# Performance work log

Measured on AMD Instinct MI355X. Metric: run time of the kernel, lower is better.

## Reference

```python
import jax, jax.numpy as jnp
import numpy as np

N = 100000
E = 3200000
F_IN, F_HID, F_OUT = 512, 16, 40


def setup_inputs() -> dict:
    key = jax.random.key(0)
    k1, k2, k3, k4 = jax.random.split(key, 4)
    x = jax.random.normal(k1, (N, F_IN), dtype=jnp.float32)
    edge_index = jax.random.randint(k2, (2, E), 0, N, dtype=jnp.int64)
    # Glorot-style init for the two GCN layer weights + zero biases
    W1 = jax.random.normal(k3, (F_IN, F_HID), dtype=jnp.float32) / np.sqrt(F_IN)
    b1 = jnp.zeros((F_HID,), dtype=jnp.float32)
    W2 = jax.random.normal(k4, (F_HID, F_OUT), dtype=jnp.float32) / np.sqrt(F_HID)
    b2 = jnp.zeros((F_OUT,), dtype=jnp.float32)
    return {"x": x, "edge_index": edge_index, "W1": W1, "b1": b1, "W2": W2, "b2": b2}


def _gcn_conv(x, src, dst, W, b):
    # x' = D^{-1/2} (A + I) D^{-1/2} (x W) + b   (standard GCNConv with self-loops)
    n = x.shape[0]
    h = x @ W  # [N, F_out] -- transform first (cheap edge traffic)
    deg = jax.ops.segment_sum(jnp.ones_like(dst, dtype=h.dtype), dst, num_segments=n) + 1.0  # +1 self-loop
    dinv = jax.lax.rsqrt(deg)
    msgs = h[src] * (dinv[src] * dinv[dst])[:, None]  # [E, F_out]
    agg = jax.ops.segment_sum(msgs, dst, num_segments=n)
    agg = agg + h * (dinv * dinv)[:, None]  # self-loop contribution
    return agg + b


def reference(x, edge_index, W1, b1, W2, b2):
    src, dst = edge_index[0], edge_index[1]
    h = _gcn_conv(x, src, dst, W1, b1)
    h = jax.nn.relu(h)
    # dropout is identity in eval mode (training=False)
    h = _gcn_conv(h, src, dst, W2, b2)
    return jax.nn.log_softmax(h, axis=1)
```

## Files before the change

kernel.cpp:

```cpp
#include <hip/hip_runtime.h>
#include <hip/hip_fp16.h>
#include <math.h>

#define FIN 512
#define FH 16
#define FOUT 40
#define DT 448
#define SUB 512
#define SRC_BITS 17
#define SRC_MASK 0x1FFFF
#define BCHUNK 4096
#define HCHUNK 16384
#define NB_MAX 1024
#define AP 17
#define NTS_MAX 200

typedef unsigned int u32;

__device__ __forceinline__ void gload_lds16(const void* g, void* l) {
  __builtin_amdgcn_global_load_lds((const __attribute__((address_space(1))) u32*)g,
                                   (__attribute__((address_space(3))) u32*)l, 16, 0, 0);
}

__global__ __launch_bounds__(256) void histA_k(const int* __restrict__ dst, int E, int NB,
                                               unsigned* __restrict__ bcnt) {
  __shared__ unsigned h[NB_MAX];
  for (int b = threadIdx.x; b < NB; b += 256) h[b] = 0;
  __syncthreads();
  const int base = blockIdx.x * HCHUNK;
  const int cn = min(HCHUNK, E - base);
  for (int u = threadIdx.x; u < cn; u += 256)
    atomicAdd(&h[((unsigned)dst[base + u]) / DT], 1u);
  __syncthreads();
  for (int b = threadIdx.x; b < NB; b += 256) {
    unsigned c = h[b];
    if (c) atomicAdd(&bcnt[b], c);
  }
}

__global__ __launch_bounds__(1024) void scanB_k(const unsigned* __restrict__ bcnt, int NB,
                                                unsigned* __restrict__ boff,
                                                unsigned* __restrict__ bcur) {
  __shared__ unsigned ws[16];
  const int t = threadIdx.x, lane = t & 63, wid = t >> 6;
  unsigned v = (t < NB) ? bcnt[t] : 0;
  unsigned incl = v;
#pragma unroll
  for (int d = 1; d < 64; d <<= 1) {
    unsigned o = __shfl_up(incl, d);
    if (lane >= d) incl += o;
  }
  if (lane == 63) ws[wid] = incl;
  __syncthreads();
  unsigned woff = 0, tot = 0;
#pragma unroll
  for (int w = 0; w < 16; ++w) {
    unsigned s = ws[w];
    if (w < wid) woff += s;
    tot += s;
  }
  unsigned ex = woff + incl - v;
  if (t < NB) { boff[t] = ex; bcur[t] = ex; }
  if (t == 0) boff[NB] = tot;
}

__global__ __launch_bounds__(256) void bin_k(const int* __restrict__ src,
                                             const int* __restrict__ dst, int E, int NB,
                                             unsigned* __restrict__ bcur,
                                             unsigned* __restrict__ bins) {
  __shared__ unsigned hist[NB_MAX];
  __shared__ unsigned excl[NB_MAX];
  __shared__ unsigned gbase[NB_MAX];
  __shared__ unsigned lcur[NB_MAX];
  __shared__ unsigned stage[BCHUNK];
  __shared__ unsigned short sbkt[BCHUNK];
  __shared__ unsigned wtot[4];
  const int t = threadIdx.x, lane = t & 63, wid = t >> 6;
  for (int b = t; b < NB; b += 256) hist[b] = 0;
  __syncthreads();
  const int base = blockIdx.x * BCHUNK;
  const int cn = min(BCHUNK, E - base);
  for (int u = t; u < cn; u += 256)
    atomicAdd(&hist[((unsigned)dst[base + u]) / DT], 1u);
  __syncthreads();
  unsigned loc[4], s = 0;
#pragma unroll
  for (int j = 0; j < 4; ++j) {
    int idx = t * 4 + j;
    loc[j] = s;
    s += (idx < NB) ? hist[idx] : 0;
  }
  unsigned incl = s;
#pragma unroll
  for (int d = 1; d < 64; d <<= 1) {
    unsigned o = __shfl_up(incl, d);
    if (lane >= d) incl += o;
  }
  if (lane == 63) wtot[wid] = incl;
  __syncthreads();
  unsigned woff = 0;
  for (int w = 0; w < wid; ++w) woff += wtot[w];
  unsigned tex = woff + incl - s;
#pragma unroll
  for (int j = 0; j < 4; ++j) {
    int idx = t * 4 + j;
    if (idx < NB) excl[idx] = tex + loc[j];
  }
  __syncthreads();
  for (int b = t; b < NB; b += 256) {
    unsigned c = hist[b];
    gbase[b] = c ? atomicAdd(&bcur[b], c) : 0u;
    lcur[b] = excl[b];
  }
  __syncthreads();
  for (int u = t; u < cn; u += 256) {
    int e = base + u;
    unsigned d = (unsigned)dst[e];
    unsigned bkt = d / DT;
    unsigned dloc = d - bkt * DT;
    unsigned pk = ((unsigned)src[e]) | (dloc << SRC_BITS);
    unsigned lr = atomicAdd(&lcur[bkt], 1u);
    stage[lr] = pk;
    sbkt[lr] = (unsigned short)bkt;
  }
  __syncthreads();
  for (int u = t; u < cn; u += 256) {
    unsigned bkt = sbkt[u];
    bins[gbase[bkt] + (u - excl[bkt])] = stage[u];
  }
}

__global__ __launch_bounds__(512) void deg_k(const unsigned* __restrict__ boff,
                                             const unsigned* __restrict__ bins, int n,
                                             float* __restrict__ dinv) {
  __shared__ unsigned dh[DT];
  const int t = threadIdx.x, b = blockIdx.x;
  if (t < DT) dh[t] = 0;
  __syncthreads();
  const unsigned jb = boff[b], je = boff[b + 1];
  for (unsigned j = jb + t; j < je; j += 512) atomicAdd(&dh[bins[j] >> SRC_BITS], 1u);
  __syncthreads();
  const int i = b * DT + t;
  if (t < DT && i < n) dinv[i] = rsqrtf((float)dh[t] + 1.0f);
}

__global__ __launch_bounds__(1024) void bin2_k(const unsigned* __restrict__ boff,
                                               const unsigned* __restrict__ bins, int nts,
                                               unsigned* __restrict__ out2,
                                               unsigned* __restrict__ off2) {
  __shared__ unsigned h2[NTS_MAX];
  __shared__ unsigned o2[NTS_MAX + 1];
  __shared__ unsigned cur2[NTS_MAX];
  const int t = threadIdx.x, b = blockIdx.x;
  const unsigned jb = boff[b], je = boff[b + 1];
  if (t < nts) h2[t] = 0;
  __syncthreads();
  for (unsigned j = jb + t; j < je; j += 1024)
    atomicAdd(&h2[(bins[j] & SRC_MASK) >> 9], 1u);
  __syncthreads();
  if (t == 0) {
    unsigned s = 0;
    for (int i = 0; i < nts; ++i) { o2[i] = s; s += h2[i]; }
    o2[nts] = s;
  }
  __syncthreads();
  if (t < nts) cur2[t] = o2[t];
  if (t <= nts) off2[(size_t)b * (nts + 1) + t] = o2[t];
  __syncthreads();
  for (unsigned j = jb + t; j < je; j += 1024) {
    const unsigned pk = bins[j];
    const unsigned srcf = pk & SRC_MASK;
    const unsigned st = srcf >> 9;
    const unsigned p = atomicAdd(&cur2[st], 1u);
    out2[jb + p] = (srcf & 511u) | ((pk >> SRC_BITS) << 9);
  }
}

__global__ __launch_bounds__(256) void gemm1_k(const float* __restrict__ x,
                                               const float* __restrict__ W1,
                                               const float* __restrict__ dinv, int n,
                                               __half* __restrict__ hs1) {
  __shared__ float w1s[FIN * FH];
  for (int idx = threadIdx.x; idx < FIN * FH; idx += 256) w1s[idx] = W1[idx];
  __syncthreads();
  const int row_raw = blockIdx.x * 256 + threadIdx.x;
  const int row = row_raw < n ? row_raw : n - 1;
  const float4* __restrict__ xr = (const float4*)(x + (size_t)row * FIN);
  float4 a0 = {0, 0, 0, 0}, a1 = {0, 0, 0, 0}, a2 = {0, 0, 0, 0}, a3 = {0, 0, 0, 0};
#pragma unroll 2
  for (int it = 0; it < FIN / 4; ++it) {
    float4 xv = xr[it];
    const float* wf = w1s + it * 4 * FH;
#pragma unroll
    for (int j = 0; j < 4; ++j) {
      const float xj = (j == 0) ? xv.x : (j == 1) ? xv.y : (j == 2) ? xv.z : xv.w;
      const float* wj = wf + j * FH;
      float4 w0 = *(const float4*)(wj + 0);
      float4 w1 = *(const float4*)(wj + 4);
      float4 w2 = *(const float4*)(wj + 8);
      float4 w3 = *(const float4*)(wj + 12);
      a0.x += xj * w0.x; a0.y += xj * w0.y; a0.z += xj * w0.z; a0.w += xj * w0.w;
      a1.x += xj * w1.x; a1.y += xj * w1.y; a1.z += xj * w1.z; a1.w += xj * w1.w;
      a2.x += xj * w2.x; a2.y += xj * w2.y; a2.z += xj * w2.z; a2.w += xj * w2.w;
      a3.x += xj * w3.x; a3.y += xj * w3.y; a3.z += xj * w3.z; a3.w += xj * w3.w;
    }
  }
  if (row_raw < n) {
    const float di = dinv[row];
    __half2 hb[8];
    hb[0] = __floats2half2_rn(a0.x * di, a0.y * di);
    hb[1] = __floats2half2_rn(a0.z * di, a0.w * di);
    hb[2] = __floats2half2_rn(a1.x * di, a1.y * di);
    hb[3] = __floats2half2_rn(a1.z * di, a1.w * di);
    hb[4] = __floats2half2_rn(a2.x * di, a2.y * di);
    hb[5] = __floats2half2_rn(a2.z * di, a2.w * di);
    hb[6] = __floats2half2_rn(a3.x * di, a3.y * di);
    hb[7] = __floats2half2_rn(a3.z * di, a3.w * di);
    uint4* o = (uint4*)(hs1 + (size_t)row * FH);
    o[0] = ((const uint4*)hb)[0];
    o[1] = ((const uint4*)hb)[1];
  }
}

__device__ __forceinline__ void accum_row(float* __restrict__ arow, uint4 q0, uint4 q1) {
  float2 f;
  f = __half22float2(*(const __half2*)&q0.x); atomicAdd(arow + 0, f.x);  atomicAdd(arow + 1, f.y);
  f = __half22float2(*(const __half2*)&q0.y); atomicAdd(arow + 2, f.x);  atomicAdd(arow + 3, f.y);
  f = __half22float2(*(const __half2*)&q0.z); atomicAdd(arow + 4, f.x);  atomicAdd(arow + 5, f.y);
  f = __half22float2(*(const __half2*)&q0.w); atomicAdd(arow + 6, f.x);  atomicAdd(arow + 7, f.y);
  f = __half22float2(*(const __half2*)&q1.x); atomicAdd(arow + 8, f.x);  atomicAdd(arow + 9, f.y);
  f = __half22float2(*(const __half2*)&q1.y); atomicAdd(arow + 10, f.x); atomicAdd(arow + 11, f.y);
  f = __half22float2(*(const __half2*)&q1.z); atomicAdd(arow + 12, f.x); atomicAdd(arow + 13, f.y);
  f = __half22float2(*(const __half2*)&q1.w); atomicAdd(arow + 14, f.x); atomicAdd(arow + 15, f.y);
}

__device__ __forceinline__ void stage_sub(const __half* __restrict__ tab, int st,
                                          __half* __restrict__ buf, int t) {
  const __half* g = tab + ((size_t)st * SUB + (t >> 1)) * FH + (t & 1) * 8;
  gload_lds16(g, buf + t * 8);
}

__device__ __forceinline__ void consume_sub(const unsigned* __restrict__ out2, unsigned jb,
                                            unsigned a, unsigned e,
                                            const __half* __restrict__ buf,
                                            float* __restrict__ acc, int t) {
  for (unsigned j = a + t; j < e; j += 1024) {
    const unsigned pk = out2[jb + j];
    const int srcl = pk & 511, dstl = pk >> 9;
    const uint4 q0 = *(const uint4*)(buf + srcl * FH);
    const uint4 q1 = *(const uint4*)(buf + srcl * FH + 8);
    accum_row(acc + dstl * AP, q0, q1);
  }
}

__device__ __forceinline__ void tile_gather(const __half* __restrict__ tab,
                                            const unsigned* __restrict__ out2,
                                            const unsigned* __restrict__ off2r,
                                            unsigned jb, int nts, int t,
                                            __half* __restrict__ sb0,
                                            __half* __restrict__ sb1,
                                            float* __restrict__ acc) {
  for (int u = t; u < DT * AP; u += 1024) acc[u] = 0.f;
  stage_sub(tab, 0, sb0, t);
  __syncthreads();
  for (int st = 0; st < nts; ++st) {
    asm volatile("s_waitcnt vmcnt(0)" ::: "memory");
    __builtin_amdgcn_sched_barrier(0);
    __builtin_amdgcn_s_barrier();
    __builtin_amdgcn_sched_barrier(0);
    __half* cur = (st & 1) ? sb1 : sb0;
    __half* nxt = (st & 1) ? sb0 : sb1;
    if (st + 1 < nts) stage_sub(tab, st + 1, nxt, t);
    consume_sub(out2, jb, off2r[st], off2r[st + 1], cur, acc, t);
    __builtin_amdgcn_sched_barrier(0);
    __builtin_amdgcn_s_barrier();
    __builtin_amdgcn_sched_barrier(0);
  }
  __syncthreads();
}

__global__ __launch_bounds__(1024) void gath1_k(const __half* __restrict__ hs1,
                                                const unsigned* __restrict__ boff,
                                                const unsigned* __restrict__ out2,
                                                const unsigned* __restrict__ off2, int nts,
                                                const float* __restrict__ dinv,
                                                const float* __restrict__ b1, int n,
                                                __half* __restrict__ rs) {
  __shared__ float acc[DT * AP];
  __shared__ __half sb0[SUB * FH];
  __shared__ __half sb1[SUB * FH];
  __shared__ float b1s[FH];
  const int t = threadIdx.x, b = blockIdx.x;
  if (t < FH) b1s[t] = b1[t];
  tile_gather(hs1, out2, off2 + (size_t)b * (nts + 1), boff[b], nts, t, sb0, sb1, acc);
  const int base = b * DT;
  for (int idx = t; idx < DT * 4; idx += 1024) {
    const int node = idx >> 2, sub = idx & 3;
    const int i = base + node;
    if (i < n) {
      const float* arow = acc + node * AP + sub * 4;
      const float a0 = arow[0], a1 = arow[1], a2 = arow[2], a3 = arow[3];
      const __half2* hp = (const __half2*)(hs1 + (size_t)i * FH + sub * 4);
      const float2 h0 = __half22float2(hp[0]);
      const float2 h1 = __half22float2(hp[1]);
      const float d = dinv[i];
      float r0 = (a0 + h0.x) * d + b1s[sub * 4 + 0];
      float r1 = (a1 + h0.y) * d + b1s[sub * 4 + 1];
      float r2 = (a2 + h1.x) * d + b1s[sub * 4 + 2];
      float r3 = (a3 + h1.y) * d + b1s[sub * 4 + 3];
      r0 = fmaxf(r0, 0.f) * d;
      r1 = fmaxf(r1, 0.f) * d;
      r2 = fmaxf(r2, 0.f) * d;
      r3 = fmaxf(r3, 0.f) * d;
      __half2* rp = (__half2*)(rs + (size_t)i * FH + sub * 4);
      rp[0] = __floats2half2_rn(r0, r1);
      rp[1] = __floats2half2_rn(r2, r3);
    }
  }
}

__global__ __launch_bounds__(1024) void gath2_k(const __half* __restrict__ rs,
                                                const unsigned* __restrict__ boff,
                                                const unsigned* __restrict__ out2,
                                                const unsigned* __restrict__ off2, int nts,
                                                const float* __restrict__ dinv,
                                                const float* __restrict__ W2,
                                                const float* __restrict__ b2, int n,
                                                float* __restrict__ out) {
  __shared__ float acc[DT * AP];
  __shared__ __half sb0[SUB * FH];
  __shared__ __half sb1[SUB * FH];
  const int t = threadIdx.x, b = blockIdx.x;
  tile_gather(rs, out2, off2 + (size_t)b * (nts + 1), boff[b], nts, t, sb0, sb1, acc);
  const int base = b * DT;
  for (int idx = t; idx < DT * 4; idx += 1024) {
    const int node = idx >> 2, sub = idx & 3;
    const int i = base + node;
    if (i < n) {
      float* arow = acc + node * AP + sub * 4;
      const __half2* rp = (const __half2*)(rs + (size_t)i * FH + sub * 4);
      const float2 r0 = __half22float2(rp[0]);
      const float2 r1 = __half22float2(rp[1]);
      const float d = dinv[i];
      arow[0] = (arow[0] + r0.x) * d;
      arow[1] = (arow[1] + r0.y) * d;
      arow[2] = (arow[2] + r1.x) * d;
      arow[3] = (arow[3] + r1.y) * d;
    }
  }
  __syncthreads();
  float* w2s = (float*)sb0;
  for (int idx = t; idx < FH * FOUT + FOUT; idx += 1024)
    w2s[idx] = (idx < FH * FOUT) ? W2[idx] : b2[idx - FH * FOUT];
  __syncthreads();
  const int lane = t & 63, wv = t >> 6;
  for (int nd = wv; nd < DT; nd += 16) {
    const int i = base + nd;
    if (i >= n) continue;
    float hv = (lane < FOUT) ? w2s[FH * FOUT + lane] : 0.f;
#pragma unroll
    for (int kk = 0; kk < 16; ++kk) {
      const float a = acc[nd * AP + kk];
      if (lane < FOUT) hv += a * w2s[kk * FOUT + lane];
    }
    float m = (lane < FOUT) ? hv : -INFINITY;
#pragma unroll
    for (int d = 1; d < 64; d <<= 1) m = fmaxf(m, __shfl_xor(m, d));
    float ex = (lane < FOUT) ? expf(hv - m) : 0.f;
#pragma unroll
    for (int d = 1; d < 64; d <<= 1) ex += __shfl_xor(ex, d);
    if (lane < FOUT) out[(size_t)i * FOUT + lane] = hv - m - logf(ex);
  }
}

extern "C" void kernel_launch(void* const* d_in, const int* in_sizes, int n_in,
                              void* d_out, int out_size, void* d_ws, size_t ws_size,
                              hipStream_t stream) {
  const float* x  = (const float*)d_in[0];
  const int*   ei = (const int*)d_in[1];
  const float* W1 = (const float*)d_in[2];
  const float* b1 = (const float*)d_in[3];
  const float* W2 = (const float*)d_in[4];
  const float* b2 = (const float*)d_in[5];
  float* out = (float*)d_out;

  const int n = in_sizes[0] / FIN;
  const int E = in_sizes[1] / 2;
  const int* src = ei;
  const int* dst = ei + E;
  const int NB  = (n + DT - 1) / DT;
  const int NTS = (n + SUB - 1) / SUB;
  const size_t padRows = (size_t)NTS * SUB;

  char* ws = (char*)d_ws;
  size_t o = 0;
  auto alloc = [&](size_t bytes) {
    void* p = ws + o;
    o = (o + bytes + 255) & ~(size_t)255;
    return p;
  };
  unsigned* bcnt = (unsigned*)alloc((size_t)(NB + 1) * 4);
  unsigned* boff = (unsigned*)alloc((size_t)(NB + 1) * 4);
  unsigned* bcur = (unsigned*)alloc((size_t)NB * 4);
  float*    dinv = (float*)alloc((size_t)n * 4);
  unsigned* bins = (unsigned*)alloc((size_t)E * 4);
  unsigned* out2 = (unsigned*)alloc((size_t)E * 4);
  unsigned* off2 = (unsigned*)alloc((size_t)NB * (NTS + 1) * 4);
  __half*   hs1  = (__half*)alloc(padRows * FH * 2);
  __half*   rsb  = (__half*)alloc(padRows * FH * 2);

  hipMemsetAsync(bcnt, 0, (size_t)(NB + 1) * 4, stream);

  histA_k<<<(E + HCHUNK - 1) / HCHUNK, 256, 0, stream>>>(dst, E, NB, bcnt);
  scanB_k<<<1, 1024, 0, stream>>>(bcnt, NB, boff, bcur);
  bin_k<<<(E + BCHUNK - 1) / BCHUNK, 256, 0, stream>>>(src, dst, E, NB, bcur, bins);
  deg_k<<<NB, 512, 0, stream>>>(boff, bins, n, dinv);
  bin2_k<<<NB, 1024, 0, stream>>>(boff, bins, NTS, out2, off2);

  gemm1_k<<<(n + 255) / 256, 256, 0, stream>>>(x, W1, dinv, n, hs1);
  gath1_k<<<NB, 1024, 0, stream>>>(hs1, boff, out2, off2, NTS, dinv, b1, n, rsb);
  gath2_k<<<NB, 1024, 0, stream>>>(rsb, boff, out2, off2, NTS, dinv, W2, b2, n, out);
}
```

Before: 909.4 us.

## Use four-slot ring of smaller source tiles with three-deep async prefetch

Halves the source sub-tile to 256 nodes and replaces the double buffer with a 4-slot LDS ring. Only 512 threads issue the async global-to-LDS loads, prefetching three tiles ahead with partial vmcnt waits, and one barrier per step is dropped. The goal is to hide gather-load latency better and cut synchronisation per tile. The cost is twice as many sub-tiles, so more barriers and offset entries in the binning pass.

Measured after the change: 1.123 ms. 1.23x slower.

```diff
diff --git a/kernel.cpp b/kernel.cpp
--- a/kernel.cpp
+++ b/kernel.cpp
@@ -6,14 +6,15 @@
 #define FH 16
 #define FOUT 40
 #define DT 448
-#define SUB 512
+#define SUB 256
+#define SUBSH 8
 #define SRC_BITS 17
 #define SRC_MASK 0x1FFFF
 #define BCHUNK 4096
 #define HCHUNK 16384
 #define NB_MAX 1024
 #define AP 17
-#define NTS_MAX 200
+#define NTS_MAX 400
 
 typedef unsigned int u32;
 
@@ -156,7 +157,7 @@
   if (t < nts) h2[t] = 0;
   __syncthreads();
   for (unsigned j = jb + t; j < je; j += 1024)
-    atomicAdd(&h2[(bins[j] & SRC_MASK) >> 9], 1u);
+    atomicAdd(&h2[(bins[j] & SRC_MASK) >> SUBSH], 1u);
   __syncthreads();
   if (t == 0) {
     unsigned s = 0;
@@ -170,9 +171,9 @@
   for (unsigned j = jb + t; j < je; j += 1024) {
     const unsigned pk = bins[j];
     const unsigned srcf = pk & SRC_MASK;
-    const unsigned st = srcf >> 9;
+    const unsigned st = srcf >> SUBSH;
     const unsigned p = atomicAdd(&cur2[st], 1u);
-    out2[jb + p] = (srcf & 511u) | ((pk >> SRC_BITS) << 9);
+    out2[jb + p] = (srcf & (SUB - 1)) | ((pk >> SRC_BITS) << SUBSH);
   }
 }
 
@@ -246,7 +247,7 @@
                                             float* __restrict__ acc, int t) {
   for (unsigned j = a + t; j < e; j += 1024) {
     const unsigned pk = out2[jb + j];
-    const int srcl = pk & 511, dstl = pk >> 9;
+    const int srcl = pk & (SUB - 1), dstl = pk >> SUBSH;
     const uint4 q0 = *(const uint4*)(buf + srcl * FH);
     const uint4 q1 = *(const uint4*)(buf + srcl * FH + 8);
     accum_row(acc + dstl * AP, q0, q1);
@@ -257,24 +258,29 @@
                                             const unsigned* __restrict__ out2,
                                             const unsigned* __restrict__ off2r,
                                             unsigned jb, int nts, int t,
-                                            __half* __restrict__ sb0,
-                                            __half* __restrict__ sb1,
+                                            __half* __restrict__ bufs,
                                             float* __restrict__ acc) {
   for (int u = t; u < DT * AP; u += 1024) acc[u] = 0.f;
-  stage_sub(tab, 0, sb0, t);
+  const bool stager = (t < 512);
+  if (stager) {
+    stage_sub(tab, 0, bufs + 0 * SUB * FH, t);
+    if (1 < nts) stage_sub(tab, 1, bufs + 1 * SUB * FH, t);
+    if (2 < nts) stage_sub(tab, 2, bufs + 2 * SUB * FH, t);
+  }
   __syncthreads();
   for (int st = 0; st < nts; ++st) {
-    asm volatile("s_waitcnt vmcnt(0)" ::: "memory");
-    __builtin_amdgcn_sched_barrier(0);
+    if (stager) {
+      const int rem = nts - 1 - st;
+      if (rem >= 2)      { asm volatile("s_waitcnt vmcnt(2)" ::: "memory"); }
+      else if (rem == 1) { asm volatile("s_waitcnt vmcnt(1)" ::: "memory"); }
+      else               { asm volatile("s_waitcnt vmcnt(0)" ::: "memory"); }
+      __builtin_amdgcn_sched_barrier(0);
+    }
     __builtin_amdgcn_s_barrier();
     __builtin_amdgcn_sched_barrier(0);
-    __half* cur = (st & 1) ? sb1 : sb0;
-    __half* nxt = (st & 1) ? sb0 : sb1;
-    if (st + 1 < nts) stage_sub(tab, st + 1, nxt, t);
-    consume_sub(out2, jb, off2r[st], off2r[st + 1], cur, acc, t);
-    __builtin_amdgcn_sched_barrier(0);
-    __builtin_amdgcn_s_barrier();
-    __builtin_amdgcn_sched_barrier(0);
+    if (stager && (st + 3) < nts)
+      stage_sub(tab, st + 3, bufs + ((st + 3) & 3) * SUB * FH, t);
+    consume_sub(out2, jb, off2r[st], off2r[st + 1], bufs + (st & 3) * SUB * FH, acc, t);
   }
   __syncthreads();
 }
@@ -287,12 +293,11 @@
                                                 const float* __restrict__ b1, int n,
                                                 __half* __restrict__ rs) {
   __shared__ float acc[DT * AP];
-  __shared__ __half sb0[SUB * FH];
-  __shared__ __half sb1[SUB * FH];
+  __shared__ __half bufs[4 * SUB * FH];
   __shared__ float b1s[FH];
   const int t = threadIdx.x, b = blockIdx.x;
   if (t < FH) b1s[t] = b1[t];
-  tile_gather(hs1, out2, off2 + (size_t)b * (nts + 1), boff[b], nts, t, sb0, sb1, acc);
+  tile_gather(hs1, out2, off2 + (size_t)b * (nts + 1), boff[b], nts, t, bufs, acc);
   const int base = b * DT;
   for (int idx = t; idx < DT * 4; idx += 1024) {
     const int node = idx >> 2, sub = idx & 3;
@@ -328,10 +333,9 @@
                                                 const float* __restrict__ b2, int n,
                                                 float* __restrict__ out) {
   __shared__ float acc[DT * AP];
-  __shared__ __half sb0[SUB * FH];
-  __shared__ __half sb1[SUB * FH];
+  __shared__ __half bufs[4 * SUB * FH];
   const int t = threadIdx.x, b = blockIdx.x;
-  tile_gather(rs, out2, off2 + (size_t)b * (nts + 1), boff[b], nts, t, sb0, sb1, acc);
+  tile_gather(rs, out2, off2 + (size_t)b * (nts + 1), boff[b], nts, t, bufs, acc);
   const int base = b * DT;
   for (int idx = t; idx < DT * 4; idx += 1024) {
     const int node = idx >> 2, sub = idx & 3;
@@ -349,7 +353,7 @@
     }
   }
   __syncthreads();
-  float* w2s = (float*)sb0;
+  float* w2s = (float*)bufs;
   for (int idx = t; idx < FH * FOUT + FOUT; idx += 1024)
     w2s[idx] = (idx < FH * FOUT) ? W2[idx] : b2[idx - FH * FOUT];
   __syncthreads();
```
